# Performance work log

Hardware: AMD Instinct MI355X
Metric: run time of the kernel (lower is better)

The kernel has to match this reference:

```python
import jax, jax.numpy as jnp
import numpy as np

N_NODES = 100000


def _gcn_layer(x, src, dst, ew, norm_s, norm_d, W, b):
    # DGL GraphConv with edge weights, norm='both':
    # h_v = D_in(v)^-1/2 * sum_{(u,v) in E} w_uv * D_out(u)^-1/2 * x_u; then Linear.
    m = (x * norm_s[:, None])[src] * ew[:, None]        # [E, d] gather + weight
    agg = jax.ops.segment_sum(m, dst, num_segments=N_NODES)  # [N, d] scatter-add
    return (agg * norm_d[:, None]) @ W + b


def setup_inputs() -> dict:
    key = jax.random.key(0)
    ks = jax.random.split(key, 12)
    N, E, D, C = N_NODES, 1600000, 64, 32
    inp = {
        "x": jax.random.normal(ks[0], (N, D), jnp.float32),
        "src": jax.random.randint(ks[1], (E,), 0, N, jnp.int64),
        "dst": jax.random.randint(ks[2], (E,), 0, N, jnp.int64),
        "ew": jax.random.uniform(ks[3], (E,), jnp.float32),
    }
    s = 1.0 / np.sqrt(D)
    for i, k in zip(range(1, 5), ks[4:8]):
        inp[f"W{i}"] = jax.random.normal(k, (D, D), jnp.float32) * s
        inp[f"b{i}"] = jnp.zeros((D,), jnp.float32)
    inp["Wr"] = jax.random.normal(ks[8], (D, D), jnp.float32) * s
    inp["br"] = jnp.zeros((D,), jnp.float32)
    inp["Wo"] = jax.random.normal(ks[9], (D, C), jnp.float32) * s
    inp["bo"] = jnp.zeros((C,), jnp.float32)
    return inp


def reference(x, src, dst, ew, W1, b1, W2, b2, W3, b3, W4, b4, Wr, br, Wo, bo):
    ones = jnp.ones(src.shape, x.dtype)
    deg_out = jnp.clip(jax.ops.segment_sum(ones, src, num_segments=N_NODES), 1.0)
    deg_in = jnp.clip(jax.ops.segment_sum(ones, dst, num_segments=N_NODES), 1.0)
    norm_s = deg_out ** -0.5
    norm_d = deg_in ** -0.5

    res = x @ Wr + br
    h = jax.nn.relu(_gcn_layer(x, src, dst, ew, norm_s, norm_d, W1, b1))
    h = jax.nn.relu(_gcn_layer(h, src, dst, ew, norm_s, norm_d, W2, b2))
    h = jax.nn.relu(_gcn_layer(h, src, dst, ew, norm_s, norm_d, W3, b3))
    h = _gcn_layer(h, src, dst, ew, norm_s, norm_d, W4, b4)
    h = jax.nn.relu(h + res)
    return h @ Wo + bo
```

## Files before the change

kernel.cpp:

```cpp
#include <hip/hip_runtime.h>

#define NN 100000
#define D 64
#define G 3
#define RS 33334
#define NC 85
#define NB (G*NC)

typedef short bf16x8 __attribute__((ext_vector_type(8)));
typedef float f32x4 __attribute__((ext_vector_type(4)));
typedef float f32x2 __attribute__((ext_vector_type(2)));

__device__ __forceinline__ float bf2f_lo(unsigned w) { return __uint_as_float(w << 16); }
__device__ __forceinline__ float bf2f_hi(unsigned w) { return __uint_as_float(w & 0xffff0000u); }
__device__ __forceinline__ unsigned short f2bf(float f) {
    unsigned u = __float_as_uint(f);
    return (unsigned short)((u + 0x7fffu + ((u >> 16) & 1u)) >> 16);
}
__device__ __forceinline__ unsigned pack2(float a, float b) {
    return (unsigned)f2bf(a) | ((unsigned)f2bf(b) << 16);
}
__device__ __forceinline__ unsigned char f2fp8(float v) {
    return (unsigned char)(__builtin_amdgcn_cvt_pk_fp8_f32(v, v, 0, false) & 0xff);
}
__device__ __forceinline__ unsigned pack_cw(int s, float w) {
    return ((unsigned)f2bf(w) << 17) | (unsigned)s;
}

__global__ __launch_bounds__(1024) void k_hist(const int* __restrict__ src,
                                               const int* __restrict__ dst,
                                               unsigned short* __restrict__ psd, int E) {
    __shared__ unsigned h[RS / 2];
    int b = blockIdx.x, t = threadIdx.x;
    int g = b / NC, c = b - g * NC;
    int lo = g * RS;
    for (int i = t; i < RS / 2; i += 1024) h[i] = 0;
    __syncthreads();
    int e0 = (int)((((long long)c * E / NC)) & ~3LL);
    int e1 = (c == NC - 1) ? E : (int)((((long long)(c + 1) * E / NC)) & ~3LL);
    int m = (e1 - e0) & ~4095;
    for (int e = e0 + t * 4; e < e0 + m; e += 4096) {
        int4 s4 = *(const int4*)(src + e);
        int4 d4 = *(const int4*)(dst + e);
        int v;
        v = s4.x - lo; if ((unsigned)v < RS) atomicAdd(&h[v >> 1], 1u << ((v & 1) * 16));
        v = s4.y - lo; if ((unsigned)v < RS) atomicAdd(&h[v >> 1], 1u << ((v & 1) * 16));
        v = s4.z - lo; if ((unsigned)v < RS) atomicAdd(&h[v >> 1], 1u << ((v & 1) * 16));
        v = s4.w - lo; if ((unsigned)v < RS) atomicAdd(&h[v >> 1], 1u << ((v & 1) * 16));
        v = d4.x - lo; if ((unsigned)v < RS) atomicAdd(&h[v >> 1], 1u << ((v & 1) * 16 + 8));
        v = d4.y - lo; if ((unsigned)v < RS) atomicAdd(&h[v >> 1], 1u << ((v & 1) * 16 + 8));
        v = d4.z - lo; if ((unsigned)v < RS) atomicAdd(&h[v >> 1], 1u << ((v & 1) * 16 + 8));
        v = d4.w - lo; if ((unsigned)v < RS) atomicAdd(&h[v >> 1], 1u << ((v & 1) * 16 + 8));
    }
    for (int e = e0 + m + t; e < e1; e += 1024) {
        int v = src[e] - lo; if ((unsigned)v < RS) atomicAdd(&h[v >> 1], 1u << ((v & 1) * 16));
        v = dst[e] - lo;     if ((unsigned)v < RS) atomicAdd(&h[v >> 1], 1u << ((v & 1) * 16 + 8));
    }
    __syncthreads();
    unsigned* pb = (unsigned*)(psd + (size_t)b * RS);
    for (int i = t; i < RS / 2; i += 1024) pb[i] = h[i];
}

__global__ __launch_bounds__(1024) void k_scan1m(const unsigned short* __restrict__ psd,
                                                 float* __restrict__ ns, float* __restrict__ nd,
                                                 int* __restrict__ rowptr,
                                                 int* __restrict__ bsum, int n) {
    __shared__ int lds[1024];
    int t = threadIdx.x;
    int i = blockIdx.x * 1024 + t;
    int sv = 0, dv = 0;
    if (i < n) {
        int g = i / RS, off = i - g * RS;
        const unsigned short* p = psd + (size_t)(g * NC) * RS + off;
        #pragma unroll 5
        for (int c = 0; c < NC; ++c) {
            unsigned v = p[(size_t)c * RS];
            sv += (int)(v & 0xffu);
            dv += (int)(v >> 8);
        }
        ns[i] = rsqrtf(fmaxf((float)sv, 1.0f));
        nd[i] = rsqrtf(fmaxf((float)dv, 1.0f));
    }
    lds[t] = dv;
    __syncthreads();
    for (int off = 1; off < 1024; off <<= 1) {
        int v = lds[t];
        int a = (t >= off) ? lds[t - off] : 0;
        __syncthreads();
        lds[t] = v + a;
        __syncthreads();
    }
    if (t == 1023) bsum[blockIdx.x] = lds[1023];
    if (i < n) rowptr[i] = lds[t] - dv;
}

__global__ void k_scan3c(int* __restrict__ rowptr, const int* __restrict__ bsum,
                         const unsigned short* __restrict__ psd,
                         unsigned short* __restrict__ cur16,
                         int n, int E, int nb) {
    __shared__ int sbs[128];
    int t = threadIdx.x;
    if (t < 128) sbs[t] = (t < nb) ? bsum[t] : 0;
    __syncthreads();
    for (int off = 1; off < 128; off <<= 1) {
        int v = 0, a = 0;
        if (t < 128) { v = sbs[t]; if (t >= off) a = sbs[t - off]; }
        __syncthreads();
        if (t < 128) sbs[t] = v + a;
        __syncthreads();
    }
    int i = blockIdx.x * blockDim.x + t;
    if (i == 0) rowptr[n] = E;
    if (i >= n) return;
    int blk = i >> 10;
    int base = (blk > 0) ? sbs[blk - 1] : 0;
    int r = rowptr[i] + base;
    rowptr[i] = r;
    int g = i / RS, off = i - g * RS;
    const unsigned short* p = psd + (size_t)(g * NC) * RS + off;
    unsigned short* cp = cur16 + (size_t)(g * NC) * RS + off;
    int run = 0;
    #pragma unroll 5
    for (int c = 0; c < NC; ++c) {
        cp[(size_t)c * RS] = (unsigned short)run;
        run += (int)(p[(size_t)c * RS] >> 8);
    }
}

__global__ __launch_bounds__(1024) void k_fillsort(const int* __restrict__ src,
                                                   const int* __restrict__ dst,
                                                   const float* __restrict__ ew,
                                                   const int* __restrict__ rowptr,
                                                   const unsigned short* __restrict__ cur16,
                                                   unsigned* __restrict__ cw, int E) {
    __shared__ int cur[RS];
    int b = blockIdx.x, t = threadIdx.x;
    int g = b / NC, c = b - g * NC;
    int lo = g * RS;
    const unsigned short* c16 = cur16 + (size_t)b * RS;
    for (int i = t; i < RS; i += 1024) cur[i] = rowptr[lo + i] + (int)c16[i];
    __syncthreads();
    int e0 = (int)((((long long)c * E / NC)) & ~3LL);
    int e1 = (c == NC - 1) ? E : (int)((((long long)(c + 1) * E / NC)) & ~3LL);
    int m = (e1 - e0) & ~4095;
    for (int e = e0 + t * 4; e < e0 + m; e += 4096) {
        int4 s4 = *(const int4*)(src + e);
        int4 d4 = *(const int4*)(dst + e);
        float4 w4 = *(const float4*)(ew + e);
        int d;
        d = d4.x - lo; if ((unsigned)d < RS) { int p = atomicAdd(&cur[d], 1); cw[p] = pack_cw(s4.x, w4.x); }
        d = d4.y - lo; if ((unsigned)d < RS) { int p = atomicAdd(&cur[d], 1); cw[p] = pack_cw(s4.y, w4.y); }
        d = d4.z - lo; if ((unsigned)d < RS) { int p = atomicAdd(&cur[d], 1); cw[p] = pack_cw(s4.z, w4.z); }
        d = d4.w - lo; if ((unsigned)d < RS) { int p = atomicAdd(&cur[d], 1); cw[p] = pack_cw(s4.w, w4.w); }
    }
    for (int e = e0 + m + t; e < e1; e += 1024) {
        int d = dst[e] - lo;
        if ((unsigned)d < RS) {
            int p = atomicAdd(&cur[d], 1);
            cw[p] = pack_cw(src[e], ew[e]);
        }
    }
}

__global__ __launch_bounds__(256) void k_gemm2(const float* __restrict__ x,
                                               const float* __restrict__ Wr,
                                               const float* __restrict__ brs,
                                               const float* __restrict__ W1,
                                               const float* __restrict__ ns,
                                               unsigned short* __restrict__ resb,
                                               unsigned char* __restrict__ tmat, int n) {
    __shared__ unsigned short WTr[64][72];
    __shared__ unsigned short WT1[64][72];
    int t = threadIdx.x;
    for (int i = t; i < 64 * 64; i += 256) {
        int k = i >> 6, nn = i & 63;
        WTr[nn][k] = f2bf(Wr[i]);
        WT1[nn][k] = f2bf(W1[i]);
    }
    __syncthreads();
    int w = t >> 6, lane = t & 63;
    int m = lane & 15, q = lane >> 4;
    int node0 = blockIdx.x * 64 + w * 16;
    int nodeA = min(node0 + m, n - 1);
    const float* inf = x + (size_t)nodeA * D;
    float sc = ns[nodeA];
    bf16x8 afr[2], afs[2];
    #pragma unroll
    for (int kc = 0; kc < 2; ++kc) {
        float4 f0 = *(const float4*)(inf + kc * 32 + q * 8);
        float4 f1 = *(const float4*)(inf + kc * 32 + q * 8 + 4);
        union { bf16x8 v; unsigned short u[8]; } ta, ts;
        ta.u[0] = f2bf(f0.x); ta.u[1] = f2bf(f0.y);
        ta.u[2] = f2bf(f0.z); ta.u[3] = f2bf(f0.w);
        ta.u[4] = f2bf(f1.x); ta.u[5] = f2bf(f1.y);
        ta.u[6] = f2bf(f1.z); ta.u[7] = f2bf(f1.w);
        ts.u[0] = f2bf(f0.x * sc); ts.u[1] = f2bf(f0.y * sc);
        ts.u[2] = f2bf(f0.z * sc); ts.u[3] = f2bf(f0.w * sc);
        ts.u[4] = f2bf(f1.x * sc); ts.u[5] = f2bf(f1.y * sc);
        ts.u[6] = f2bf(f1.z * sc); ts.u[7] = f2bf(f1.w * sc);
        afr[kc] = ta.v;
        afs[kc] = ts.v;
    }
    #pragma unroll
    for (int nt = 0; nt < 4; ++nt) {
        f32x4 ar = {0.f, 0.f, 0.f, 0.f};
        f32x4 at = {0.f, 0.f, 0.f, 0.f};
        #pragma unroll
        for (int kc = 0; kc < 2; ++kc) {
            union { bf16x8 v; uint4 u; } bfr, bf1;
            bfr.u = *(const uint4*)&WTr[nt * 16 + m][kc * 32 + q * 8];
            bf1.u = *(const uint4*)&WT1[nt * 16 + m][kc * 32 + q * 8];
            ar = __builtin_amdgcn_mfma_f32_16x16x32_bf16(afr[kc], bfr.v, ar, 0, 0, 0);
            at = __builtin_amdgcn_mfma_f32_16x16x32_bf16(afs[kc], bf1.v, at, 0, 0, 0);
        }
        int col = nt * 16 + m;
        float bb = brs[col];
        #pragma unroll
        for (int r = 0; r < 4; ++r) {
            int node = node0 + q * 4 + r;
            if (node < n) {
                resb[(size_t)node * D + col] = f2bf(ar[r] + bb);
                tmat[(size_t)node * D + col] = f2fp8(at[r]);
            }
        }
    }
}

template<int OUTD, bool LAST>
__global__ __launch_bounds__(256) void k_gg(const int* __restrict__ rowptr,
                                            const unsigned* __restrict__ cw,
                                            const unsigned char* __restrict__ tmat,
                                            const float* __restrict__ nd,
                                            const float* __restrict__ ns,
                                            const float* __restrict__ bg,
                                            const unsigned short* __restrict__ resb,
                                            const float* __restrict__ W,
                                            const float* __restrict__ bo,
                                            void* __restrict__ out_, int n, int E) {
    __shared__ unsigned short HT[64][72];
    __shared__ unsigned short WT[OUTD][72];
    int t = threadIdx.x;
    for (int i = t; i < 64 * OUTD; i += 256) {
        int k = i / OUTD, nn = i % OUTD;
        WT[nn][k] = f2bf(W[i]);
    }
    int hw = t >> 5;
    int lane = t & 31;
    int g = lane >> 3;
    int h = lane & 7;
    int base = blockIdx.x * 64;
    for (int p = 0; p < 8; ++p) {
        int nl = hw * 8 + p;
        int node = base + nl;
        float v0 = 0, v1 = 0, v2 = 0, v3 = 0, v4 = 0, v5 = 0, v6 = 0, v7 = 0;
        if (node < n) {
            int beg = rowptr[node], end = rowptr[node + 1];
            float a0=0,a1=0,a2=0,a3=0,a4=0,a5=0,a6=0,a7=0;
            float c0=0,c1=0,c2=0,c3=0,c4=0,c5=0,c6=0,c7=0;
            for (int eb = beg; eb < end; eb += 16) {
                int eA = eb + g;
                int eB = eA + 4;
                int eC = eA + 8;
                int eD = eA + 12;
                unsigned cvA = cw[min(eA, E - 1)];
                unsigned cvB = cw[min(eB, E - 1)];
                unsigned cvC = cw[min(eC, E - 1)];
                unsigned cvD = cw[min(eD, E - 1)];
                float wA = (eA < end) ? __uint_as_float((cvA >> 17) << 16) : 0.f;
                float wB = (eB < end) ? __uint_as_float((cvB >> 17) << 16) : 0.f;
                float wC = (eC < end) ? __uint_as_float((cvC >> 17) << 16) : 0.f;
                float wD = (eD < end) ? __uint_as_float((cvD >> 17) << 16) : 0.f;
                uint2 rA = *((const uint2*)(tmat + (size_t)(cvA & 0x1FFFFu) * D) + h);
                uint2 rB = *((const uint2*)(tmat + (size_t)(cvB & 0x1FFFFu) * D) + h);
                uint2 rC = *((const uint2*)(tmat + (size_t)(cvC & 0x1FFFFu) * D) + h);
                uint2 rD = *((const uint2*)(tmat + (size_t)(cvD & 0x1FFFFu) * D) + h);
                f32x2 p0, p1, p2, p3;
                p0 = __builtin_amdgcn_cvt_pk_f32_fp8(rA.x, false);
                p1 = __builtin_amdgcn_cvt_pk_f32_fp8(rA.x, true);
                p2 = __builtin_amdgcn_cvt_pk_f32_fp8(rA.y, false);
                p3 = __builtin_amdgcn_cvt_pk_f32_fp8(rA.y, true);
                a0 += wA * p0.x; a1 += wA * p0.y; a2 += wA * p1.x; a3 += wA * p1.y;
                a4 += wA * p2.x; a5 += wA * p2.y; a6 += wA * p3.x; a7 += wA * p3.y;
                p0 = __builtin_amdgcn_cvt_pk_f32_fp8(rB.x, false);
                p1 = __builtin_amdgcn_cvt_pk_f32_fp8(rB.x, true);
                p2 = __builtin_amdgcn_cvt_pk_f32_fp8(rB.y, false);
                p3 = __builtin_amdgcn_cvt_pk_f32_fp8(rB.y, true);
                c0 += wB * p0.x; c1 += wB * p0.y; c2 += wB * p1.x; c3 += wB * p1.y;
                c4 += wB * p2.x; c5 += wB * p2.y; c6 += wB * p3.x; c7 += wB * p3.y;
                p0 = __builtin_amdgcn_cvt_pk_f32_fp8(rC.x, false);
                p1 = __builtin_amdgcn_cvt_pk_f32_fp8(rC.x, true);
                p2 = __builtin_amdgcn_cvt_pk_f32_fp8(rC.y, false);
                p3 = __builtin_amdgcn_cvt_pk_f32_fp8(rC.y, true);
                a0 += wC * p0.x; a1 += wC * p0.y; a2 += wC * p1.x; a3 += wC * p1.y;
                a4 += wC * p2.x; a5 += wC * p2.y; a6 += wC * p3.x; a7 += wC * p3.y;
                p0 = __builtin_amdgcn_cvt_pk_f32_fp8(rD.x, false);
                p1 = __builtin_amdgcn_cvt_pk_f32_fp8(rD.x, true);
                p2 = __builtin_amdgcn_cvt_pk_f32_fp8(rD.y, false);
                p3 = __builtin_amdgcn_cvt_pk_f32_fp8(rD.y, true);
                c0 += wD * p0.x; c1 += wD * p0.y; c2 += wD * p1.x; c3 += wD * p1.y;
                c4 += wD * p2.x; c5 += wD * p2.y; c6 += wD * p3.x; c7 += wD * p3.y;
            }
            a0 += c0; a1 += c1; a2 += c2; a3 += c3;
            a4 += c4; a5 += c5; a6 += c6; a7 += c7;
            #pragma unroll
            for (int msk = 8; msk <= 16; msk <<= 1) {
                a0 += __shfl_xor(a0, msk); a1 += __shfl_xor(a1, msk);
                a2 += __shfl_xor(a2, msk); a3 += __shfl_xor(a3, msk);
                a4 += __shfl_xor(a4, msk); a5 += __shfl_xor(a5, msk);
                a6 += __shfl_xor(a6, msk); a7 += __shfl_xor(a7, msk);
            }
            float ndv = nd[node];
            float4 b0 = *(const float4*)(bg + 8 * h);
            float4 b1 = *(const float4*)(bg + 8 * h + 4);
            v0 = ndv * a0 + b0.x; v1 = ndv * a1 + b0.y;
            v2 = ndv * a2 + b0.z; v3 = ndv * a3 + b0.w;
            v4 = ndv * a4 + b1.x; v5 = ndv * a5 + b1.y;
            v6 = ndv * a6 + b1.z; v7 = ndv * a7 + b1.w;
            if (LAST) {
                uint4 r = *((const uint4*)(resb + (size_t)node * D) + h);
                v0 += bf2f_lo(r.x); v1 += bf2f_hi(r.x);
                v2 += bf2f_lo(r.y); v3 += bf2f_hi(r.y);
                v4 += bf2f_lo(r.z); v5 += bf2f_hi(r.z);
                v6 += bf2f_lo(r.w); v7 += bf2f_hi(r.w);
            }
            v0 = fmaxf(v0, 0.f); v1 = fmaxf(v1, 0.f); v2 = fmaxf(v2, 0.f); v3 = fmaxf(v3, 0.f);
            v4 = fmaxf(v4, 0.f); v5 = fmaxf(v5, 0.f); v6 = fmaxf(v6, 0.f); v7 = fmaxf(v7, 0.f);
            if (!LAST) {
                float s = ns[node];
                v0 *= s; v1 *= s; v2 *= s; v3 *= s; v4 *= s; v5 *= s; v6 *= s; v7 *= s;
            }
        }
        if (g == 0) {
            *((uint4*)&HT[nl][8 * h]) =
                make_uint4(pack2(v0, v1), pack2(v2, v3), pack2(v4, v5), pack2(v6, v7));
        }
    }
    __syncthreads();
    int w = t >> 6, l64 = t & 63;
    int m = l64 & 15, q = l64 >> 4;
    int row0 = w * 16;
    bf16x8 afr[2];
    #pragma unroll
    for (int kc = 0; kc < 2; ++kc) {
        union { bf16x8 v; uint4 u; } tmp;
        tmp.u = *(const uint4*)&HT[row0 + m][kc * 32 + q * 8];
        afr[kc] = tmp.v;
    }
    constexpr int NT = OUTD / 16;
    #pragma unroll
    for (int nt = 0; nt < NT; ++nt) {
        f32x4 acc = {0.f, 0.f, 0.f, 0.f};
        #pragma unroll
        for (int kc = 0; kc < 2; ++kc) {
            union { bf16x8 v; uint4 u; } bfr;
            bfr.u = *(const uint4*)&WT[nt * 16 + m][kc * 32 + q * 8];
            acc = __builtin_amdgcn_mfma_f32_16x16x32_bf16(afr[kc], bfr.v, acc, 0, 0, 0);
        }
        int col = nt * 16 + m;
        float bb = LAST ? bo[col] : 0.f;
        #pragma unroll
        for (int r = 0; r < 4; ++r) {
            int node = base + row0 + q * 4 + r;
            if (node < n) {
                float v = acc[r] + bb;
                if (LAST)
                    ((float*)out_)[(size_t)node * OUTD + col] = v;
                else
                    ((unsigned char*)out_)[(size_t)node * OUTD + col] = f2fp8(v);
            }
        }
    }
}

static inline char* align_up(char* p, size_t a) {
    return (char*)(((uintptr_t)p + a - 1) & ~(uintptr_t)(a - 1));
}

extern "C" void kernel_launch(void* const* d_in, const int* in_sizes, int n_in,
                              void* d_out, int out_size, void* d_ws, size_t ws_size,
                              hipStream_t stream) {
    const float* x   = (const float*)d_in[0];
    const int*   src = (const int*)d_in[1];
    const int*   dst = (const int*)d_in[2];
    const float* ew  = (const float*)d_in[3];
    const float* Wl[4] = {(const float*)d_in[4], (const float*)d_in[6],
                          (const float*)d_in[8], (const float*)d_in[10]};
    const float* bl[4] = {(const float*)d_in[5], (const float*)d_in[7],
                          (const float*)d_in[9], (const float*)d_in[11]};
    const float* Wr = (const float*)d_in[12];
    const float* br = (const float*)d_in[13];
    const float* Wo = (const float*)d_in[14];
    const float* bo = (const float*)d_in[15];
    float* out = (float*)d_out;

    const int N = NN;
    const int E = in_sizes[1];

    char* p = (char*)d_ws;
    float* norm_s = (float*)p;            p = align_up(p + N * 4, 256);
    float* norm_d = (float*)p;            p = align_up(p + N * 4, 256);
    int*   rowptr = (int*)p;              p = align_up(p + (size_t)(G * RS + 80) * 4, 256);
    int*   bsum   = (int*)p;              p = align_up(p + 128 * 4, 256);
    unsigned* cw  = (unsigned*)p;         p = align_up(p + (size_t)E * 4, 256);
    unsigned short* psd   = (unsigned short*)p; p = align_up(p + (size_t)NB * RS * 2, 256);
    unsigned short* cur16 = (unsigned short*)p; p = align_up(p + (size_t)NB * RS * 2, 256);
    unsigned short* resb  = (unsigned short*)p; p = align_up(p + (size_t)N * D * 2, 256);
    unsigned char* tA = (unsigned char*)psd;
    unsigned char* tB = tA + (size_t)N * D;

    k_hist<<<NB, 1024, 0, stream>>>(src, dst, psd, E);
    int nb = (N + 1023) / 1024;
    k_scan1m<<<nb, 1024, 0, stream>>>(psd, norm_s, norm_d, rowptr, bsum, N);
    k_scan3c<<<(N + 255) / 256, 256, 0, stream>>>(rowptr, bsum, psd, cur16, N, E, nb);
    k_fillsort<<<NB, 1024, 0, stream>>>(src, dst, ew, rowptr, cur16, cw, E);

    k_gemm2<<<(N + 63) / 64, 256, 0, stream>>>(x, Wr, br, Wl[0], norm_s, resb, tA, N);

    k_gg<64, false><<<(N + 63) / 64, 256, 0, stream>>>(
        rowptr, cw, tA, norm_d, norm_s, bl[0], nullptr, Wl[1], nullptr, tB, N, E);
    k_gg<64, false><<<(N + 63) / 64, 256, 0, stream>>>(
        rowptr, cw, tB, norm_d, norm_s, bl[1], nullptr, Wl[2], nullptr, tA, N, E);
    k_gg<64, false><<<(N + 63) / 64, 256, 0, stream>>>(
        rowptr, cw, tA, norm_d, norm_s, bl[2], nullptr, Wl[3], nullptr, tB, N, E);
    k_gg<32, true><<<(N + 63) / 64, 256, 0, stream>>>(
        rowptr, cw, tB, norm_d, nullptr, bl[3], resb, Wo, bo, out, N, E);
}
```

Baseline: 354.8 us.

## Split fused gather+GEMM kernel into separate gather and GEMM kernels

Each fused gather-then-GEMM layer kernel is replaced by a standalone gather kernel, launched with one 32-lane group per node and 8 nodes per block, plus a separate MFMA GEMM kernel. The two communicate through a bf16 intermediate buffer in global memory. The aim is finer-grained, better load-balanced scheduling of the irregular gather, with no per-block barrier and no LDS staging. In exchange it adds extra kernel launches and a global write and read of an N x 64 bf16 array per layer.

Result: faster. 329.7 us (-7.1%).

```diff
diff --git a/kernel.cpp b/kernel.cpp
--- a/kernel.cpp
+++ b/kernel.cpp
@@ -226,127 +226,124 @@
     }
 }
 
-template<int OUTD, bool LAST>
-__global__ __launch_bounds__(256) void k_gg(const int* __restrict__ rowptr,
-                                            const unsigned* __restrict__ cw,
-                                            const unsigned char* __restrict__ tmat,
-                                            const float* __restrict__ nd,
-                                            const float* __restrict__ ns,
-                                            const float* __restrict__ bg,
-                                            const unsigned short* __restrict__ resb,
-                                            const float* __restrict__ W,
-                                            const float* __restrict__ bo,
-                                            void* __restrict__ out_, int n, int E) {
-    __shared__ unsigned short HT[64][72];
+template<bool LAST>
+__global__ void k_gather(const int* __restrict__ rowptr, const unsigned* __restrict__ cw,
+                         const unsigned char* __restrict__ tmat,
+                         const float* __restrict__ nd, const float* __restrict__ ns,
+                         const float* __restrict__ bias,
+                         const unsigned short* __restrict__ resb,
+                         unsigned short* __restrict__ outb, int n, int E) {
+    int node = blockIdx.x * (blockDim.x >> 5) + (threadIdx.x >> 5);
+    int lane = threadIdx.x & 31;
+    if (node >= n) return;
+    int g = lane >> 3;
+    int h = lane & 7;
+    int beg = rowptr[node], end = rowptr[node + 1];
+    float a0=0,a1=0,a2=0,a3=0,a4=0,a5=0,a6=0,a7=0;
+    float c0=0,c1=0,c2=0,c3=0,c4=0,c5=0,c6=0,c7=0;
+    for (int base = beg; base < end; base += 16) {
+        int eA = base + g;
+        int eB = eA + 4;
+        int eC = eA + 8;
+        int eD = eA + 12;
+        unsigned cvA = cw[min(eA, E - 1)];
+        unsigned cvB = cw[min(eB, E - 1)];
+        unsigned cvC = cw[min(eC, E - 1)];
+        unsigned cvD = cw[min(eD, E - 1)];
+        float wA = (eA < end) ? __uint_as_float((cvA >> 17) << 16) : 0.f;
+        float wB = (eB < end) ? __uint_as_float((cvB >> 17) << 16) : 0.f;
+        float wC = (eC < end) ? __uint_as_float((cvC >> 17) << 16) : 0.f;
+        float wD = (eD < end) ? __uint_as_float((cvD >> 17) << 16) : 0.f;
+        uint2 rA = *((const uint2*)(tmat + (size_t)(cvA & 0x1FFFFu) * D) + h);
+        uint2 rB = *((const uint2*)(tmat + (size_t)(cvB & 0x1FFFFu) * D) + h);
+        uint2 rC = *((const uint2*)(tmat + (size_t)(cvC & 0x1FFFFu) * D) + h);
+        uint2 rD = *((const uint2*)(tmat + (size_t)(cvD & 0x1FFFFu) * D) + h);
+        f32x2 p0, p1, p2, p3;
+        p0 = __builtin_amdgcn_cvt_pk_f32_fp8(rA.x, false);
+        p1 = __builtin_amdgcn_cvt_pk_f32_fp8(rA.x, true);
+        p2 = __builtin_amdgcn_cvt_pk_f32_fp8(rA.y, false);
+        p3 = __builtin_amdgcn_cvt_pk_f32_fp8(rA.y, true);
+        a0 += wA * p0.x; a1 += wA * p0.y; a2 += wA * p1.x; a3 += wA * p1.y;
+        a4 += wA * p2.x; a5 += wA * p2.y; a6 += wA * p3.x; a7 += wA * p3.y;
+        p0 = __builtin_amdgcn_cvt_pk_f32_fp8(rB.x, false);
+        p1 = __builtin_amdgcn_cvt_pk_f32_fp8(rB.x, true);
+        p2 = __builtin_amdgcn_cvt_pk_f32_fp8(rB.y, false);
+        p3 = __builtin_amdgcn_cvt_pk_f32_fp8(rB.y, true);
+        c0 += wB * p0.x; c1 += wB * p0.y; c2 += wB * p1.x; c3 += wB * p1.y;
+        c4 += wB * p2.x; c5 += wB * p2.y; c6 += wB * p3.x; c7 += wB * p3.y;
+        p0 = __builtin_amdgcn_cvt_pk_f32_fp8(rC.x, false);
+        p1 = __builtin_amdgcn_cvt_pk_f32_fp8(rC.x, true);
+        p2 = __builtin_amdgcn_cvt_pk_f32_fp8(rC.y, false);
+        p3 = __builtin_amdgcn_cvt_pk_f32_fp8(rC.y, true);
+        a0 += wC * p0.x; a1 += wC * p0.y; a2 += wC * p1.x; a3 += wC * p1.y;
+        a4 += wC * p2.x; a5 += wC * p2.y; a6 += wC * p3.x; a7 += wC * p3.y;
+        p0 = __builtin_amdgcn_cvt_pk_f32_fp8(rD.x, false);
+        p1 = __builtin_amdgcn_cvt_pk_f32_fp8(rD.x, true);
+        p2 = __builtin_amdgcn_cvt_pk_f32_fp8(rD.y, false);
+        p3 = __builtin_amdgcn_cvt_pk_f32_fp8(rD.y, true);
+        c0 += wD * p0.x; c1 += wD * p0.y; c2 += wD * p1.x; c3 += wD * p1.y;
+        c4 += wD * p2.x; c5 += wD * p2.y; c6 += wD * p3.x; c7 += wD * p3.y;
+    }
+    a0 += c0; a1 += c1; a2 += c2; a3 += c3;
+    a4 += c4; a5 += c5; a6 += c6; a7 += c7;
+    #pragma unroll
+    for (int msk = 8; msk <= 16; msk <<= 1) {
+        a0 += __shfl_xor(a0, msk); a1 += __shfl_xor(a1, msk);
+        a2 += __shfl_xor(a2, msk); a3 += __shfl_xor(a3, msk);
+        a4 += __shfl_xor(a4, msk); a5 += __shfl_xor(a5, msk);
+        a6 += __shfl_xor(a6, msk); a7 += __shfl_xor(a7, msk);
+    }
+    float ndv = nd[node];
+    float4 b0 = *(const float4*)(bias + 8 * h);
+    float4 b1 = *(const float4*)(bias + 8 * h + 4);
+    float v0 = ndv * a0 + b0.x, v1 = ndv * a1 + b0.y;
+    float v2 = ndv * a2 + b0.z, v3 = ndv * a3 + b0.w;
+    float v4 = ndv * a4 + b1.x, v5 = ndv * a5 + b1.y;
+    float v6 = ndv * a6 + b1.z, v7 = ndv * a7 + b1.w;
+    if (LAST) {
+        uint4 r = *((const uint4*)(resb + (size_t)node * D) + h);
+        v0 += bf2f_lo(r.x); v1 += bf2f_hi(r.x);
+        v2 += bf2f_lo(r.y); v3 += bf2f_hi(r.y);
+        v4 += bf2f_lo(r.z); v5 += bf2f_hi(r.z);
+        v6 += bf2f_lo(r.w); v7 += bf2f_hi(r.w);
+    }
+    v0 = fmaxf(v0, 0.f); v1 = fmaxf(v1, 0.f); v2 = fmaxf(v2, 0.f); v3 = fmaxf(v3, 0.f);
+    v4 = fmaxf(v4, 0.f); v5 = fmaxf(v5, 0.f); v6 = fmaxf(v6, 0.f); v7 = fmaxf(v7, 0.f);
+    if (!LAST) {
+        float s = ns[node];
+        v0 *= s; v1 *= s; v2 *= s; v3 *= s; v4 *= s; v5 *= s; v6 *= s; v7 *= s;
+    }
+    if (g == 0) {
+        uint4 o = make_uint4(pack2(v0, v1), pack2(v2, v3), pack2(v4, v5), pack2(v6, v7));
+        *((uint4*)(outb + (size_t)node * D) + h) = o;
+    }
+}
+
+template<int OUTD, bool BIAS, int OUTMODE>
+__global__ __launch_bounds__(256) void k_gemm(const unsigned short* __restrict__ inb,
+                                              const float* __restrict__ W,
+                                              const float* __restrict__ bias,
+                                              void* __restrict__ out_, int n) {
+    constexpr int NT = OUTD / 16;
     __shared__ unsigned short WT[OUTD][72];
     int t = threadIdx.x;
     for (int i = t; i < 64 * OUTD; i += 256) {
         int k = i / OUTD, nn = i % OUTD;
         WT[nn][k] = f2bf(W[i]);
     }
-    int hw = t >> 5;
-    int lane = t & 31;
-    int g = lane >> 3;
-    int h = lane & 7;
-    int base = blockIdx.x * 64;
-    for (int p = 0; p < 8; ++p) {
-        int nl = hw * 8 + p;
-        int node = base + nl;
-        float v0 = 0, v1 = 0, v2 = 0, v3 = 0, v4 = 0, v5 = 0, v6 = 0, v7 = 0;
-        if (node < n) {
-            int beg = rowptr[node], end = rowptr[node + 1];
-            float a0=0,a1=0,a2=0,a3=0,a4=0,a5=0,a6=0,a7=0;
-            float c0=0,c1=0,c2=0,c3=0,c4=0,c5=0,c6=0,c7=0;
-            for (int eb = beg; eb < end; eb += 16) {
-                int eA = eb + g;
-                int eB = eA + 4;
-                int eC = eA + 8;
-                int eD = eA + 12;
-                unsigned cvA = cw[min(eA, E - 1)];
-                unsigned cvB = cw[min(eB, E - 1)];
-                unsigned cvC = cw[min(eC, E - 1)];
-                unsigned cvD = cw[min(eD, E - 1)];
-                float wA = (eA < end) ? __uint_as_float((cvA >> 17) << 16) : 0.f;
-                float wB = (eB < end) ? __uint_as_float((cvB >> 17) << 16) : 0.f;
-                float wC = (eC < end) ? __uint_as_float((cvC >> 17) << 16) : 0.f;
-                float wD = (eD < end) ? __uint_as_float((cvD >> 17) << 16) : 0.f;
-                uint2 rA = *((const uint2*)(tmat + (size_t)(cvA & 0x1FFFFu) * D) + h);
-                uint2 rB = *((const uint2*)(tmat + (size_t)(cvB & 0x1FFFFu) * D) + h);
-                uint2 rC = *((const uint2*)(tmat + (size_t)(cvC & 0x1FFFFu) * D) + h);
-                uint2 rD = *((const uint2*)(tmat + (size_t)(cvD & 0x1FFFFu) * D) + h);
-                f32x2 p0, p1, p2, p3;
-                p0 = __builtin_amdgcn_cvt_pk_f32_fp8(rA.x, false);
-                p1 = __builtin_amdgcn_cvt_pk_f32_fp8(rA.x, true);
-                p2 = __builtin_amdgcn_cvt_pk_f32_fp8(rA.y, false);
-                p3 = __builtin_amdgcn_cvt_pk_f32_fp8(rA.y, true);
-                a0 += wA * p0.x; a1 += wA * p0.y; a2 += wA * p1.x; a3 += wA * p1.y;
-                a4 += wA * p2.x; a5 += wA * p2.y; a6 += wA * p3.x; a7 += wA * p3.y;
-                p0 = __builtin_amdgcn_cvt_pk_f32_fp8(rB.x, false);
-                p1 = __builtin_amdgcn_cvt_pk_f32_fp8(rB.x, true);
-                p2 = __builtin_amdgcn_cvt_pk_f32_fp8(rB.y, false);
-                p3 = __builtin_amdgcn_cvt_pk_f32_fp8(rB.y, true);
-                c0 += wB * p0.x; c1 += wB * p0.y; c2 += wB * p1.x; c3 += wB * p1.y;
-                c4 += wB * p2.x; c5 += wB * p2.y; c6 += wB * p3.x; c7 += wB * p3.y;
-                p0 = __builtin_amdgcn_cvt_pk_f32_fp8(rC.x, false);
-                p1 = __builtin_amdgcn_cvt_pk_f32_fp8(rC.x, true);
-                p2 = __builtin_amdgcn_cvt_pk_f32_fp8(rC.y, false);
-                p3 = __builtin_amdgcn_cvt_pk_f32_fp8(rC.y, true);
-                a0 += wC * p0.x; a1 += wC * p0.y; a2 += wC * p1.x; a3 += wC * p1.y;
-                a4 += wC * p2.x; a5 += wC * p2.y; a6 += wC * p3.x; a7 += wC * p3.y;
-                p0 = __builtin_amdgcn_cvt_pk_f32_fp8(rD.x, false);
-                p1 = __builtin_amdgcn_cvt_pk_f32_fp8(rD.x, true);
-                p2 = __builtin_amdgcn_cvt_pk_f32_fp8(rD.y, false);
-                p3 = __builtin_amdgcn_cvt_pk_f32_fp8(rD.y, true);
-                c0 += wD * p0.x; c1 += wD * p0.y; c2 += wD * p1.x; c3 += wD * p1.y;
-                c4 += wD * p2.x; c5 += wD * p2.y; c6 += wD * p3.x; c7 += wD * p3.y;
-            }
-            a0 += c0; a1 += c1; a2 += c2; a3 += c3;
-            a4 += c4; a5 += c5; a6 += c6; a7 += c7;
-            #pragma unroll
-            for (int msk = 8; msk <= 16; msk <<= 1) {
-                a0 += __shfl_xor(a0, msk); a1 += __shfl_xor(a1, msk);
-                a2 += __shfl_xor(a2, msk); a3 += __shfl_xor(a3, msk);
-                a4 += __shfl_xor(a4, msk); a5 += __shfl_xor(a5, msk);
-                a6 += __shfl_xor(a6, msk); a7 += __shfl_xor(a7, msk);
-            }
-            float ndv = nd[node];
-            float4 b0 = *(const float4*)(bg + 8 * h);
-            float4 b1 = *(const float4*)(bg + 8 * h + 4);
-            v0 = ndv * a0 + b0.x; v1 = ndv * a1 + b0.y;
-            v2 = ndv * a2 + b0.z; v3 = ndv * a3 + b0.w;
-            v4 = ndv * a4 + b1.x; v5 = ndv * a5 + b1.y;
-            v6 = ndv * a6 + b1.z; v7 = ndv * a7 + b1.w;
-            if (LAST) {
-                uint4 r = *((const uint4*)(resb + (size_t)node * D) + h);
-                v0 += bf2f_lo(r.x); v1 += bf2f_hi(r.x);
-                v2 += bf2f_lo(r.y); v3 += bf2f_hi(r.y);
-                v4 += bf2f_lo(r.z); v5 += bf2f_hi(r.z);
-                v6 += bf2f_lo(r.w); v7 += bf2f_hi(r.w);
-            }
-            v0 = fmaxf(v0, 0.f); v1 = fmaxf(v1, 0.f); v2 = fmaxf(v2, 0.f); v3 = fmaxf(v3, 0.f);
-            v4 = fmaxf(v4, 0.f); v5 = fmaxf(v5, 0.f); v6 = fmaxf(v6, 0.f); v7 = fmaxf(v7, 0.f);
-            if (!LAST) {
-                float s = ns[node];
-                v0 *= s; v1 *= s; v2 *= s; v3 *= s; v4 *= s; v5 *= s; v6 *= s; v7 *= s;
-            }
-        }
-        if (g == 0) {
-            *((uint4*)&HT[nl][8 * h]) =
-                make_uint4(pack2(v0, v1), pack2(v2, v3), pack2(v4, v5), pack2(v6, v7));
-        }
-    }
-    __syncthreads();
-    int w = t >> 6, l64 = t & 63;
-    int m = l64 & 15, q = l64 >> 4;
-    int row0 = w * 16;
+    __syncthreads();
+    int w = t >> 6, lane = t & 63;
+    int m = lane & 15, q = lane >> 4;
+    int node0 = blockIdx.x * 64 + w * 16;
+    int nodeA = min(node0 + m, n - 1);
+    const unsigned short* ip = inb + (size_t)nodeA * D;
     bf16x8 afr[2];
     #pragma unroll
     for (int kc = 0; kc < 2; ++kc) {
         union { bf16x8 v; uint4 u; } tmp;
-        tmp.u = *(const uint4*)&HT[row0 + m][kc * 32 + q * 8];
+        tmp.u = *(const uint4*)(ip + kc * 32 + q * 8);
         afr[kc] = tmp.v;
     }
-    constexpr int NT = OUTD / 16;
     #pragma unroll
     for (int nt = 0; nt < NT; ++nt) {
         f32x4 acc = {0.f, 0.f, 0.f, 0.f};
@@ -357,16 +354,16 @@
             acc = __builtin_amdgcn_mfma_f32_16x16x32_bf16(afr[kc], bfr.v, acc, 0, 0, 0);
         }
         int col = nt * 16 + m;
-        float bb = LAST ? bo[col] : 0.f;
+        float bb = BIAS ? bias[col] : 0.f;
         #pragma unroll
         for (int r = 0; r < 4; ++r) {
-            int node = base + row0 + q * 4 + r;
+            int node = node0 + q * 4 + r;
             if (node < n) {
                 float v = acc[r] + bb;
-                if (LAST)
+                if (OUTMODE == 2)
+                    ((unsigned char*)out_)[(size_t)node * OUTD + col] = f2fp8(v);
+                else
                     ((float*)out_)[(size_t)node * OUTD + col] = v;
-                else
-                    ((unsigned char*)out_)[(size_t)node * OUTD + col] = f2fp8(v);
             }
         }
     }
@@ -405,8 +402,8 @@
     unsigned short* psd   = (unsigned short*)p; p = align_up(p + (size_t)NB * RS * 2, 256);
     unsigned short* cur16 = (unsigned short*)p; p = align_up(p + (size_t)NB * RS * 2, 256);
     unsigned short* resb  = (unsigned short*)p; p = align_up(p + (size_t)N * D * 2, 256);
-    unsigned char* tA = (unsigned char*)psd;
-    unsigned char* tB = tA + (size_t)N * D;
+    unsigned short* xs   = psd;
+    unsigned char*  tmat = (unsigned char*)(xs + (size_t)N * D);
 
     k_hist<<<NB, 1024, 0, stream>>>(src, dst, psd, E);
     int nb = (N + 1023) / 1024;
@@ -414,14 +411,18 @@
     k_scan3c<<<(N + 255) / 256, 256, 0, stream>>>(rowptr, bsum, psd, cur16, N, E, nb);
     k_fillsort<<<NB, 1024, 0, stream>>>(src, dst, ew, rowptr, cur16, cw, E);
 
-    k_gemm2<<<(N + 63) / 64, 256, 0, stream>>>(x, Wr, br, Wl[0], norm_s, resb, tA, N);
-
-    k_gg<64, false><<<(N + 63) / 64, 256, 0, stream>>>(
-        rowptr, cw, tA, norm_d, norm_s, bl[0], nullptr, Wl[1], nullptr, tB, N, E);
-    k_gg<64, false><<<(N + 63) / 64, 256, 0, stream>>>(
-        rowptr, cw, tB, norm_d, norm_s, bl[1], nullptr, Wl[2], nullptr, tA, N, E);
-    k_gg<64, false><<<(N + 63) / 64, 256, 0, stream>>>(
-        rowptr, cw, tA, norm_d, norm_s, bl[2], nullptr, Wl[3], nullptr, tB, N, E);
-    k_gg<32, true><<<(N + 63) / 64, 256, 0, stream>>>(
-        rowptr, cw, tB, norm_d, nullptr, bl[3], resb, Wo, bo, out, N, E);
-}
+    k_gemm2<<<(N + 63) / 64, 256, 0, stream>>>(x, Wr, br, Wl[0], norm_s, resb, tmat, N);
+
+    k_gather<false><<<(N + 7) / 8, 256, 0, stream>>>(
+        rowptr, cw, tmat, norm_d, norm_s, bl[0], nullptr, xs, N, E);
+    k_gemm<64, false, 2><<<(N + 63) / 64, 256, 0, stream>>>(xs, Wl[1], nullptr, tmat, N);
+    k_gather<false><<<(N + 7) / 8, 256, 0, stream>>>(
+        rowptr, cw, tmat, norm_d, norm_s, bl[1], nullptr, xs, N, E);
+    k_gemm<64, false, 2><<<(N + 63) / 64, 256, 0, stream>>>(xs, Wl[2], nullptr, tmat, N);
+    k_gather<false><<<(N + 7) / 8, 256, 0, stream>>>(
+        rowptr, cw, tmat, norm_d, norm_s, bl[2], nullptr, xs, N, E);
+    k_gemm<64, false, 2><<<(N + 63) / 64, 256, 0, stream>>>(xs, Wl[3], nullptr, tmat, N);
+    k_gather<true><<<(N + 7) / 8, 256, 0, stream>>>(
+        rowptr, cw, tmat, norm_d, nullptr, bl[3], resb, xs, N, E);
+    k_gemm<32, true, 0><<<(N + 63) / 64, 256, 0, stream>>>(xs, Wo, bo, out, N);
+}
```
